# Performance work log

Hardware: AMD Instinct MI355X
Metric: run time of the kernel (lower is better)

The kernel has to match this reference:

```python
import jax, jax.numpy as jnp
import numpy as np

N_NODES = 100000
N_EDGES = 1600000
F_IN = 512
D_EMB = 128
D_HID = 64
N_CLS = 32
EPS = 1e-5


def setup_inputs() -> dict:
    key = jax.random.key(0)
    ks = jax.random.split(key, 16)
    def w(k, shape):
        fan_in = shape[0]
        return jax.random.normal(k, shape, dtype=jnp.float32) / jnp.sqrt(jnp.float32(fan_in))
    return {
        "x": jax.random.normal(ks[0], (N_NODES, F_IN), dtype=jnp.float32),
        "W1": w(ks[1], (F_IN, D_EMB)), "b1": jnp.zeros((D_EMB,), jnp.float32),
        "Wc1": w(ks[2], (D_EMB, D_HID)), "bc1": jnp.zeros((D_HID,), jnp.float32),
        "Wc2": w(ks[3], (D_HID, D_HID)), "bc2": jnp.zeros((D_HID,), jnp.float32),
        "Wc3": w(ks[4], (D_HID, D_HID)), "bc3": jnp.zeros((D_HID,), jnp.float32),
        "gamma": jnp.ones((D_HID,), jnp.float32), "beta": jnp.zeros((D_HID,), jnp.float32),
        "W2": w(ks[5], (D_HID, N_CLS)), "b2": jnp.zeros((N_CLS,), jnp.float32),
        "W3": w(ks[6], (N_CLS, N_CLS)), "b3": jnp.zeros((N_CLS,), jnp.float32),
        "edge_index": jax.random.randint(ks[7], (2, N_EDGES), 0, N_NODES, dtype=jnp.int32),
    }


def _agg_mean(h, src, dst, n):
    # gather source-node features along edges, sum into destination nodes, divide by degree
    s = jax.ops.segment_sum(h[src], dst, num_segments=n)          # [N, d]
    deg = jax.ops.segment_sum(jnp.ones((src.shape[0], 1), h.dtype), dst, num_segments=n)
    return s / jnp.maximum(deg, 1.0)


def _conv1p(h, src, dst, W, b):
    # ConvolutionalLayer_1P: neighborhood gather/aggregate -> linear -> relu
    return jax.nn.relu(_agg_mean(h, src, dst, h.shape[0]) @ W + b)


def reference(x, W1, b1, Wc1, bc1, Wc2, bc2, Wc3, bc3, gamma, beta, W2, b2, W3, b3, edge_index):
    src, dst = edge_index[0], edge_index[1]
    # linmaps1 on 0th-order ptensors == identity copy
    h = jax.nn.relu(x @ W1 + b1)                 # lin1 + relu (dropout = identity in eval)
    h = _conv1p(h, src, dst, Wc1, bc1)           # conv1
    h = _conv1p(h, src, dst, Wc2, bc2)           # conv2
    h = _conv1p(h, src, dst, Wc3, bc3)           # conv3
    mean = jnp.mean(h, axis=0)
    var = jnp.var(h, axis=0)
    h = (h - mean) * jax.lax.rsqrt(var + EPS) * gamma + beta  # batchnorm (batch stats)
    h = jax.nn.relu(h @ W2 + b2)                 # lin2 + relu (dropout = identity)
    out = h @ W3 + b3                            # lin3; linmaps0 == identity
    return out
```

## Files before the change

kernel.cpp:

```cpp
#include <hip/hip_runtime.h>
#include <cstdint>
#include <cstddef>

constexpr int F_IN  = 512;
constexpr int D_EMB = 128;
constexpr int D_HID = 64;
constexpr int N_CLS = 32;

typedef __attribute__((ext_vector_type(8))) short short8;
typedef __attribute__((ext_vector_type(4))) float floatx4;

__device__ inline unsigned short f2bf(float f) {
  union { float f; uint32_t u; } v; v.f = f;
  uint32_t r = v.u + 0x7FFF + ((v.u >> 16) & 1);
  return (unsigned short)(r >> 16);
}

__global__ __launch_bounds__(256) void wt_kernel(
    const float* __restrict__ W1, short8* __restrict__ Wt2)
{
  int idx = blockIdx.x * 256 + threadIdx.x;
  int kc8 = idx >> 10, lin = idx & 1023;
  int ct = lin >> 7, rem = lin & 127, ks = rem >> 6, ln = rem & 63;
  int col = ct * 16 + (ln & 15);
  int k0 = kc8 * 64 + ks * 32 + (ln >> 4) * 8;
  short8 s;
#pragma unroll
  for (int j = 0; j < 8; ++j)
    s[j] = (short)f2bf(W1[(size_t)(k0 + j) * D_EMB + col]);
  Wt2[idx] = s;
}

__global__ __launch_bounds__(256) void l1c1_kernel(
    const float* __restrict__ X, const short8* __restrict__ Wt2,
    const float* __restrict__ b1, const float* __restrict__ Wc1,
    float* __restrict__ P, int n)
{
  __shared__ __align__(16) char smem[50176];
  short8* Xs = (short8*)smem;
  short8* Ws = (short8*)(smem + 8192);
  float (*Hs)[132] = (float(*)[132])smem;
  float (*Wc)[64]  = (float(*)[64])(smem + 33792);

  const int t = threadIdx.x;
  const int wave = t >> 6, lane = t & 63;
  const int quad = lane >> 4, mrow = lane & 15;
  const int node0 = blockIdx.x * 64;
  const int cw = wave * 2;

  float4 wp[4];
#pragma unroll
  for (int i = 0; i < 4; ++i) wp[i] = ((const float4*)Wc1)[i * 256 + t];

  const float* sp[2];
  int soff[2];
#pragma unroll
  for (int i = 0; i < 2; ++i) {
    int g = t + i * 256;
    int row = g >> 3, col8 = g & 7;
    soff[i] = row * 128 + ((col8 * 16) ^ ((row & 7) << 4));
    int gr = node0 + row; if (gr >= n) gr = n - 1;
    sp[i] = &X[(size_t)gr * F_IN + col8 * 8];
  }

  floatx4 acc[4][2];
#pragma unroll
  for (int i = 0; i < 4; ++i)
#pragma unroll
    for (int j = 0; j < 2; ++j) acc[i][j] = (floatx4){0.f, 0.f, 0.f, 0.f};

  float4 xr[2][2];
  short8 wr[4];

#pragma unroll
  for (int i = 0; i < 2; ++i) {
    xr[i][0] = *(const float4*)sp[i];
    xr[i][1] = *(const float4*)(sp[i] + 4);
  }
#pragma unroll
  for (int i = 0; i < 4; ++i) wr[i] = Wt2[t + i * 256];

  for (int kc8 = 0; kc8 < 8; ++kc8) {
    short8 s8[2];
#pragma unroll
    for (int i = 0; i < 2; ++i) {
      s8[i][0] = (short)f2bf(xr[i][0].x); s8[i][1] = (short)f2bf(xr[i][0].y);
      s8[i][2] = (short)f2bf(xr[i][0].z); s8[i][3] = (short)f2bf(xr[i][0].w);
      s8[i][4] = (short)f2bf(xr[i][1].x); s8[i][5] = (short)f2bf(xr[i][1].y);
      s8[i][6] = (short)f2bf(xr[i][1].z); s8[i][7] = (short)f2bf(xr[i][1].w);
    }
    __syncthreads();
#pragma unroll
    for (int i = 0; i < 2; ++i)
      *(short8*)((char*)Xs + soff[i]) = s8[i];
#pragma unroll
    for (int i = 0; i < 4; ++i)
      Ws[t + i * 256] = wr[i];
    __syncthreads();

    if (kc8 < 7) {
#pragma unroll
      for (int i = 0; i < 2; ++i) {
        const float* p = sp[i] + (kc8 + 1) * 64;
        xr[i][0] = *(const float4*)p;
        xr[i][1] = *(const float4*)(p + 4);
      }
#pragma unroll
      for (int i = 0; i < 4; ++i)
        wr[i] = Wt2[(kc8 + 1) * 1024 + t + i * 256];
    }

#pragma unroll
    for (int ks = 0; ks < 2; ++ks) {
      short8 af[4], bf[2];
#pragma unroll
      for (int rt = 0; rt < 4; ++rt) {
        int row = rt * 16 + mrow;
        int byteoff = row * 128 + ((ks * 64 + quad * 16) ^ ((row & 7) << 4));
        af[rt] = *(const short8*)((const char*)Xs + byteoff);
      }
#pragma unroll
      for (int c = 0; c < 2; ++c)
        bf[c] = Ws[((cw + c) * 2 + ks) * 64 + lane];
#pragma unroll
      for (int rt = 0; rt < 4; ++rt)
#pragma unroll
        for (int c = 0; c < 2; ++c)
          acc[rt][c] = __builtin_amdgcn_mfma_f32_16x16x32_bf16(
              af[rt], bf[c], acc[rt][c], 0, 0, 0);
    }
  }

  __syncthreads();
#pragma unroll
  for (int ct = 0; ct < 2; ++ct) {
    int col = (cw + ct) * 16 + mrow;
    float b = b1[col];
#pragma unroll
    for (int rt = 0; rt < 4; ++rt)
#pragma unroll
      for (int r = 0; r < 4; ++r)
        Hs[rt * 16 + quad * 4 + r][col] = fmaxf(acc[rt][ct][r] + b, 0.f);
  }
#pragma unroll
  for (int i = 0; i < 4; ++i)
    ((float4*)&Wc[0][0])[i * 256 + t] = wp[i];
  __syncthreads();

#pragma unroll
  for (int i = 0; i < 4; ++i)
    wp[i] = ((const float4*)Wc1)[1024 + i * 256 + t];

  const int rg = t >> 4, cg = t & 15;
  float acc2[4][4];
#pragma unroll
  for (int i = 0; i < 4; ++i)
#pragma unroll
    for (int j = 0; j < 4; ++j) acc2[i][j] = 0.f;

#pragma unroll 8
  for (int k = 0; k < 64; ++k) {
    float a[4] = {Hs[rg*4+0][k], Hs[rg*4+1][k], Hs[rg*4+2][k], Hs[rg*4+3][k]};
    float4 b = *(const float4*)&Wc[k][cg * 4];
#pragma unroll
    for (int i = 0; i < 4; ++i) {
      acc2[i][0] += a[i]*b.x; acc2[i][1] += a[i]*b.y;
      acc2[i][2] += a[i]*b.z; acc2[i][3] += a[i]*b.w;
    }
  }
  __syncthreads();
#pragma unroll
  for (int i = 0; i < 4; ++i)
    ((float4*)&Wc[0][0])[i * 256 + t] = wp[i];
  __syncthreads();

#pragma unroll 8
  for (int k = 0; k < 64; ++k) {
    float a[4] = {Hs[rg*4+0][64+k], Hs[rg*4+1][64+k],
                  Hs[rg*4+2][64+k], Hs[rg*4+3][64+k]};
    float4 b = *(const float4*)&Wc[k][cg * 4];
#pragma unroll
    for (int i = 0; i < 4; ++i) {
      acc2[i][0] += a[i]*b.x; acc2[i][1] += a[i]*b.y;
      acc2[i][2] += a[i]*b.z; acc2[i][3] += a[i]*b.w;
    }
  }
#pragma unroll
  for (int i = 0; i < 4; ++i) {
    int gn = node0 + rg * 4 + i;
    if (gn < n) {
      float4 o = make_float4(acc2[i][0], acc2[i][1], acc2[i][2], acc2[i][3]);
      *(float4*)&P[(size_t)gn * 64 + cg * 4] = o;
    }
  }
}

__global__ __launch_bounds__(512) void gmm_kernel(
    const float* __restrict__ P, const int* __restrict__ offs,
    const int* __restrict__ adj, const int* __restrict__ deg,
    const float* __restrict__ bin, const float* __restrict__ W,
    float* __restrict__ Out, int n)
{
  __shared__ float Hs[64][68];
  __shared__ float Ws[64][64];
  const int t = threadIdx.x;
  const int wave = t >> 6, lane = t & 63;
  const int node0 = blockIdx.x * 64;

#pragma unroll
  for (int i = 0; i < 2; ++i) {
    int lin = t + i * 512;
    ((float4*)&Ws[0][0])[lin] = ((const float4*)W)[lin];
  }
  const float bb = bin[lane];

#pragma unroll 1
  for (int nd = 0; nd < 8; ++nd) {
    int ln = wave * 8 + nd;
    int node = node0 + ln;
    float v = 0.f;
    if (node < n) {
      int beg = offs[node], end = offs[node + 1];
      float a0 = 0.f, a1 = 0.f, a2 = 0.f, a3 = 0.f;
      int j = beg;
      while (j < end) {
        int m = min(end - j, 64);
        int idx = (lane < m) ? adj[j + lane] : 0;
        int q = 0;
        for (; q + 3 < m; q += 4) {
          int s0 = __shfl(idx, q, 64),     s1 = __shfl(idx, q + 1, 64);
          int s2 = __shfl(idx, q + 2, 64), s3 = __shfl(idx, q + 3, 64);
          a0 += P[(size_t)s0 * 64 + lane];
          a1 += P[(size_t)s1 * 64 + lane];
          a2 += P[(size_t)s2 * 64 + lane];
          a3 += P[(size_t)s3 * 64 + lane];
        }
        for (; q < m; ++q) {
          int s0 = __shfl(idx, q, 64);
          a0 += P[(size_t)s0 * 64 + lane];
        }
        j += m;
      }
      float rd = 1.f / fmaxf((float)deg[node], 1.f);
      v = fmaxf(((a0 + a2) + (a1 + a3)) * rd + bb, 0.f);
    }
    Hs[ln][lane] = v;
  }
  __syncthreads();

  const int rg = t >> 4, cg = t & 15;
  float acc[2][4];
#pragma unroll
  for (int i = 0; i < 2; ++i)
#pragma unroll
    for (int j = 0; j < 4; ++j) acc[i][j] = 0.f;

#pragma unroll 8
  for (int k = 0; k < 64; ++k) {
    float a[2] = {Hs[rg * 2 + 0][k], Hs[rg * 2 + 1][k]};
    float4 b = *(const float4*)&Ws[k][cg * 4];
#pragma unroll
    for (int i = 0; i < 2; ++i) {
      acc[i][0] += a[i]*b.x; acc[i][1] += a[i]*b.y;
      acc[i][2] += a[i]*b.z; acc[i][3] += a[i]*b.w;
    }
  }
#pragma unroll
  for (int i = 0; i < 2; ++i) {
    int gn = node0 + rg * 2 + i;
    if (gn < n) {
      float4 o = make_float4(acc[i][0], acc[i][1], acc[i][2], acc[i][3]);
      *(float4*)&Out[(size_t)gn * 64 + cg * 4] = o;
    }
  }
}

__global__ __launch_bounds__(512) void gp_kernel(
    const float* __restrict__ P, const int* __restrict__ offs,
    const int* __restrict__ adj, const int* __restrict__ deg,
    const float* __restrict__ bc3, float* __restrict__ H4,
    float* __restrict__ stats, int n)
{
  const int t = threadIdx.x;
  const int wave = t >> 6, lane = t & 63;
  const int node0 = blockIdx.x * 64;
  const float bb = bc3[lane];
  float s = 0.f, s2 = 0.f;

#pragma unroll 1
  for (int nd = 0; nd < 8; ++nd) {
    int node = node0 + wave * 8 + nd;
    if (node >= n) break;
    int beg = offs[node], end = offs[node + 1];
    float a0 = 0.f, a1 = 0.f, a2 = 0.f, a3 = 0.f;
    int j = beg;
    while (j < end) {
      int m = min(end - j, 64);
      int idx = (lane < m) ? adj[j + lane] : 0;
      int q = 0;
      for (; q + 3 < m; q += 4) {
        int s0 = __shfl(idx, q, 64),      s1 = __shfl(idx, q + 1, 64);
        int s2i = __shfl(idx, q + 2, 64), s3 = __shfl(idx, q + 3, 64);
        a0 += P[(size_t)s0 * 64 + lane];
        a1 += P[(size_t)s1 * 64 + lane];
        a2 += P[(size_t)s2i * 64 + lane];
        a3 += P[(size_t)s3 * 64 + lane];
      }
      for (; q < m; ++q) {
        int s0 = __shfl(idx, q, 64);
        a0 += P[(size_t)s0 * 64 + lane];
      }
      j += m;
    }
    float rd = 1.f / fmaxf((float)deg[node], 1.f);
    float v = fmaxf(((a0 + a2) + (a1 + a3)) * rd + bb, 0.f);
    H4[(size_t)node * 64 + lane] = v;
    s += v; s2 += v * v;
  }

  __shared__ float red[2][8][64];
  red[0][wave][lane] = s; red[1][wave][lane] = s2;
  __syncthreads();
  if (t < 128) {
    int which = t >> 6, ff = t & 63;
    float a = 0.f;
#pragma unroll
    for (int w = 0; w < 8; ++w) a += red[which][w][ff];
    atomicAdd(&stats[which * 64 + ff], a);
  }
}

__global__ __launch_bounds__(256) void hist_kernel(
    const int* __restrict__ dst, int* __restrict__ G,
    float* __restrict__ stats, int nE, int B, int NB)
{
  __shared__ int h[256];
  int blk = blockIdx.x, t = threadIdx.x;
  if (blk == 0 && t < 128) stats[t] = 0.f;
  h[t] = 0;
  __syncthreads();
  int base = blk * 8192;
  int lim = min(8192, nE - base);
  for (int i = t; i < lim; i += 256)
    atomicAdd(&h[dst[base + i] >> 9], 1);
  __syncthreads();
  if (t < NB) G[t * B + blk] = h[t];
}

__global__ __launch_bounds__(256) void scan1_kernel(
    const int* __restrict__ in, int* __restrict__ out,
    int* __restrict__ bsum, int n)
{
  __shared__ int sh[256];
  int t = threadIdx.x;
  int i = blockIdx.x * 256 + t;
  int c = (i < n) ? in[i] : 0;
  sh[t] = c;
  __syncthreads();
#pragma unroll
  for (int off = 1; off < 256; off <<= 1) {
    int v = 0;
    if (t >= off) v = sh[t - off];
    __syncthreads();
    if (t >= off) sh[t] += v;
    __syncthreads();
  }
  if (i < n) out[i] = sh[t] - c;
  if (t == 255) bsum[blockIdx.x] = sh[255];
}

__global__ __launch_bounds__(256) void scan2_kernel(int* __restrict__ bsum, int nb)
{
  __shared__ int sh[256];
  __shared__ int carry;
  int t = threadIdx.x;
  if (t == 0) carry = 0;
  __syncthreads();
  for (int base = 0; base < nb; base += 256) {
    int i = base + t;
    int v = (i < nb) ? bsum[i] : 0;
    sh[t] = v;
    __syncthreads();
#pragma unroll
    for (int off = 1; off < 256; off <<= 1) {
      int u = 0;
      if (t >= off) u = sh[t - off];
      __syncthreads();
      if (t >= off) sh[t] += u;
      __syncthreads();
    }
    int c0 = carry;
    int incl = sh[t], total = sh[255];
    if (i < nb) bsum[i] = c0 + incl - v;
    __syncthreads();
    if (t == 0) carry = c0 + total;
    __syncthreads();
  }
  if (t == 0) bsum[nb] = carry;
}

__global__ __launch_bounds__(256) void scatter2_kernel(
    const int* __restrict__ src, const int* __restrict__ dst,
    const int* __restrict__ W, const int* __restrict__ bsum,
    int2* __restrict__ EP, int nE, int B, int NB)
{
  __shared__ int cur[256];
  int blk = blockIdx.x, t = threadIdx.x;
  if (t < NB) {
    int gi = t * B + blk;
    cur[t] = W[gi] + bsum[gi >> 8];
  }
  __syncthreads();
  int base = blk * 8192;
  int lim = min(8192, nE - base);
  for (int i = t; i < lim; i += 256) {
    int s = src[base + i], d = dst[base + i];
    int slot = atomicAdd(&cur[d >> 9], 1);
    EP[slot] = make_int2(s, d);
  }
}

__global__ __launch_bounds__(256) void fillc_kernel(
    const int2* __restrict__ EP, const int* __restrict__ W,
    const int* __restrict__ bsum,
    int* __restrict__ cnt, int* __restrict__ offs, int* __restrict__ adj,
    int n, int nE, int B, int NB)
{
  __shared__ int h[512];
  int b = blockIdx.x, t = threadIdx.x;
  int g0i = b * B;
  int segStart = W[g0i] + bsum[g0i >> 8];
  int segEnd = (b == NB - 1) ? nE : (W[g0i + B] + bsum[(g0i + B) >> 8]);
  int nodeBase = b << 9;

  h[t] = 0; h[t + 256] = 0;
  __syncthreads();
  for (int i = segStart + t; i < segEnd; i += 256)
    atomicAdd(&h[EP[i].y - nodeBase], 1);
  __syncthreads();
  int c0 = h[t], c1 = h[t + 256];
#pragma unroll
  for (int off = 1; off < 512; off <<= 1) {
    int a = (t >= off) ? h[t - off] : 0;
    int bb = (t + 256 >= off) ? h[t + 256 - off] : 0;
    __syncthreads();
    h[t] += a; h[t + 256] += bb;
    __syncthreads();
  }
  int e0 = h[t] - c0, e1 = h[t + 256] - c1;
  int g0 = nodeBase + t, g1 = nodeBase + t + 256;
  if (g0 < n) { cnt[g0] = c0; offs[g0] = segStart + e0; }
  if (g1 < n) { cnt[g1] = c1; offs[g1] = segStart + e1; }
  if (b == 0 && t == 0) offs[n] = nE;
  __syncthreads();
  h[t] = e0; h[t + 256] = e1;
  __syncthreads();
  for (int i = segStart + t; i < segEnd; i += 256) {
    int2 p = EP[i];
    int slot = atomicAdd(&h[p.y - nodeBase], 1);
    adj[segStart + slot] = p.x;
  }
}

__global__ __launch_bounds__(256) void fold_kernel(
    const float* __restrict__ stats, const float* __restrict__ gamma,
    const float* __restrict__ beta, const float* __restrict__ W2,
    const float* __restrict__ b2, float* __restrict__ W2f,
    float* __restrict__ b2f, int n)
{
  __shared__ float rsg[64], corr[64];
  int t = threadIdx.x;
  if (t < 64) {
    float m = stats[t] / (float)n;
    float var = stats[64 + t] / (float)n - m * m;
    float rs = rsqrtf(var + 1e-5f);
    float g = gamma[t] * rs;
    rsg[t] = g;
    corr[t] = beta[t] - m * g;
  }
  __syncthreads();
#pragma unroll
  for (int i = 0; i < 8; ++i) {
    int lin = t + i * 256;
    int k = lin >> 5;
    W2f[lin] = rsg[k] * W2[lin];
  }
  if (t < 32) {
    float a = b2[t];
    for (int k = 0; k < 64; ++k) a += corr[k] * W2[k * 32 + t];
    b2f[t] = a;
  }
}

__global__ __launch_bounds__(256) void final_kernel(
    const float* __restrict__ H4, const float* __restrict__ W2f,
    const float* __restrict__ b2f, const float* __restrict__ W3,
    const float* __restrict__ b3, float* __restrict__ Out, int n)
{
  __shared__ float Hs[64][68];
  __shared__ float W2s[64][32];
  __shared__ float W3s[32][32];
  __shared__ float Us[64][36];
  __shared__ float b2s[32], b3s[32];
  const int t = threadIdx.x;
  const int node0 = blockIdx.x * 64;

#pragma unroll
  for (int i = 0; i < 4; ++i) {
    int lin = t + i * 256;
    int node = lin >> 4, kq = lin & 15;
    float4 v = make_float4(0.f, 0.f, 0.f, 0.f);
    if (node0 + node < n)
      v = *(const float4*)&H4[(size_t)(node0 + node) * 64 + kq * 4];
    *(float4*)&Hs[node][kq * 4] = v;
  }
#pragma unroll
  for (int i = 0; i < 2; ++i) {
    int lin = t + i * 256;
    ((float4*)&W2s[0][0])[lin] = ((const float4*)W2f)[lin];
  }
  ((float4*)&W3s[0][0])[t & 255] = ((const float4*)W3)[t & 255];
  if (t < 32) { b2s[t] = b2f[t]; b3s[t] = b3[t]; }
  __syncthreads();

  const int rg = t >> 4, cg = t & 15;
  float acc[4][2] = {{0.f,0.f},{0.f,0.f},{0.f,0.f},{0.f,0.f}};
#pragma unroll 8
  for (int k = 0; k < 64; ++k) {
    float a[4] = {Hs[rg*4+0][k], Hs[rg*4+1][k], Hs[rg*4+2][k], Hs[rg*4+3][k]};
    float w0 = W2s[k][cg*2], w1 = W2s[k][cg*2+1];
#pragma unroll
    for (int i = 0; i < 4; ++i) { acc[i][0] += a[i]*w0; acc[i][1] += a[i]*w1; }
  }
#pragma unroll
  for (int i = 0; i < 4; ++i) {
    Us[rg*4+i][cg*2+0] = fmaxf(acc[i][0] + b2s[cg*2+0], 0.f);
    Us[rg*4+i][cg*2+1] = fmaxf(acc[i][1] + b2s[cg*2+1], 0.f);
  }
  __syncthreads();

  float acc2[4][2] = {{0.f,0.f},{0.f,0.f},{0.f,0.f},{0.f,0.f}};
#pragma unroll
  for (int k = 0; k < 32; ++k) {
    float a[4] = {Us[rg*4+0][k], Us[rg*4+1][k], Us[rg*4+2][k], Us[rg*4+3][k]};
    float w0 = W3s[k][cg*2], w1 = W3s[k][cg*2+1];
#pragma unroll
    for (int i = 0; i < 4; ++i) { acc2[i][0] += a[i]*w0; acc2[i][1] += a[i]*w1; }
  }
  float (*Os)[36] = (float(*)[36])Hs;
#pragma unroll
  for (int i = 0; i < 4; ++i) {
    Os[rg*4+i][cg*2+0] = acc2[i][0] + b3s[cg*2+0];
    Os[rg*4+i][cg*2+1] = acc2[i][1] + b3s[cg*2+1];
  }
  __syncthreads();
#pragma unroll
  for (int i = 0; i < 2; ++i) {
    int lin = t + i * 256;
    int node = lin >> 3, c4 = lin & 7;
    if (node0 + node < n)
      *(float4*)&Out[(size_t)(node0 + node) * 32 + c4 * 4] =
          *(float4*)&Os[node][c4 * 4];
  }
}

extern "C" void kernel_launch(void* const* d_in, const int* in_sizes, int n_in,
                              void* d_out, int out_size, void* d_ws, size_t ws_size,
                              hipStream_t stream)
{
  const float* X     = (const float*)d_in[0];
  const float* W1    = (const float*)d_in[1];
  const float* b1    = (const float*)d_in[2];
  const float* Wc1   = (const float*)d_in[3];
  const float* bc1   = (const float*)d_in[4];
  const float* Wc2   = (const float*)d_in[5];
  const float* bc2   = (const float*)d_in[6];
  const float* Wc3   = (const float*)d_in[7];
  const float* bc3   = (const float*)d_in[8];
  const float* gamma = (const float*)d_in[9];
  const float* beta  = (const float*)d_in[10];
  const float* W2    = (const float*)d_in[11];
  const float* b2    = (const float*)d_in[12];
  const float* W3    = (const float*)d_in[13];
  const float* b3    = (const float*)d_in[14];
  const int*   ei    = (const int*)d_in[15];

  const int n  = in_sizes[0] / F_IN;
  const int nE = in_sizes[15] / 2;
  const int* src  = ei;
  const int* dstv = ei + nE;

  const int NB = (n + 511) >> 9;
  const int B  = (nE + 8191) >> 13;
  const int NG = NB * B;
  const int nbG = (NG + 255) / 256;

  float* ws    = (float*)d_ws;
  float* Pa    = ws;
  float* Pb    = Pa + (size_t)n * D_HID;
  float* stats = Pb + (size_t)n * D_HID;
  float* W2f   = stats + 128;
  float* b2f   = W2f + 2048;
  int*   cnt   = (int*)(b2f + 32);
  int*   offs  = cnt + n;
  int*   G     = offs + n + 1;
  int*   W     = G + NG;
  int*   bsum  = W + NG + 1;
  int*   adj   = bsum + nbG + 1;
  uintptr_t epAddr = ((uintptr_t)(adj + nE) + 7) & ~(uintptr_t)7;
  int2*  EP    = (int2*)epAddr;
  short8* Wt2  = (short8*)(EP + nE);
  float* H4    = Pb;

  const int nb  = (n + 63) / 64;

  wt_kernel<<<32, 256, 0, stream>>>(W1, Wt2);
  l1c1_kernel<<<nb, 256, 0, stream>>>(X, Wt2, b1, Wc1, Pa, n);

  hist_kernel<<<B, 256, 0, stream>>>(dstv, G, stats, nE, B, NB);
  scan1_kernel<<<nbG, 256, 0, stream>>>(G, W, bsum, NG);
  scan2_kernel<<<1, 256, 0, stream>>>(bsum, nbG);
  scatter2_kernel<<<B, 256, 0, stream>>>(src, dstv, W, bsum, EP, nE, B, NB);
  fillc_kernel<<<NB, 256, 0, stream>>>(EP, W, bsum, cnt, offs, adj, n, nE, B, NB);

  gmm_kernel<<<nb, 512, 0, stream>>>(Pa, offs, adj, cnt, bc1, Wc2, Pb, n);

  gmm_kernel<<<nb, 512, 0, stream>>>(Pb, offs, adj, cnt, bc2, Wc3, Pa, n);

  gp_kernel<<<nb, 512, 0, stream>>>(Pa, offs, adj, cnt, bc3, H4, stats, n);

  fold_kernel<<<1, 256, 0, stream>>>(stats, gamma, beta, W2, b2, W2f, b2f, n);
  final_kernel<<<nb, 256, 0, stream>>>(H4, W2f, b2f, W3, b3, (float*)d_out, n);
}
```

Baseline: 657.8 us.

## Double-buffer lin1 GEMM prefetch and unroll neighbor gather with scalar index loads

The lin1 bf16 MFMA GEMM now keeps two register prefetch buffers, so global loads for K-chunk k+2 are issued while chunk k is computed, which hides more load latency at the cost of extra registers. The neighbor-aggregation loops in gmm_kernel and gp_kernel are replaced by a shared gather_row helper. It reads edge indices as wave-uniform values through readfirstlane on the offsets, and keeps eight independent loads in flight with a masked tail instead of using shuffles. This removes shuffle overhead and raises memory-level parallelism in the gathers, but the tail block can issue up to seven redundant loads.

```diff
diff --git a/kernel.cpp b/kernel.cpp
--- a/kernel.cpp
+++ b/kernel.cpp
@@ -69,18 +69,23 @@
 #pragma unroll
     for (int j = 0; j < 2; ++j) acc[i][j] = (floatx4){0.f, 0.f, 0.f, 0.f};
 
-  float4 xr[2][2];
-  short8 wr[4];
+  float4 xrA[2][2], xrB[2][2];
+  short8 wrA[4], wrB[4];
 
 #pragma unroll
   for (int i = 0; i < 2; ++i) {
-    xr[i][0] = *(const float4*)sp[i];
-    xr[i][1] = *(const float4*)(sp[i] + 4);
-  }
-#pragma unroll
-  for (int i = 0; i < 4; ++i) wr[i] = Wt2[t + i * 256];
-
-  for (int kc8 = 0; kc8 < 8; ++kc8) {
+    xrA[i][0] = *(const float4*)sp[i];
+    xrA[i][1] = *(const float4*)(sp[i] + 4);
+    xrB[i][0] = *(const float4*)(sp[i] + 64);
+    xrB[i][1] = *(const float4*)(sp[i] + 68);
+  }
+#pragma unroll
+  for (int i = 0; i < 4; ++i) {
+    wrA[i] = Wt2[t + i * 256];
+    wrB[i] = Wt2[1024 + t + i * 256];
+  }
+
+  auto substep = [&](float4 (&xr)[2][2], short8 (&wr)[4], int knext) {
     short8 s8[2];
 #pragma unroll
     for (int i = 0; i < 2; ++i) {
@@ -98,16 +103,16 @@
       Ws[t + i * 256] = wr[i];
     __syncthreads();
 
-    if (kc8 < 7) {
+    if (knext < 8) {
 #pragma unroll
       for (int i = 0; i < 2; ++i) {
-        const float* p = sp[i] + (kc8 + 1) * 64;
+        const float* p = sp[i] + knext * 64;
         xr[i][0] = *(const float4*)p;
         xr[i][1] = *(const float4*)(p + 4);
       }
 #pragma unroll
       for (int i = 0; i < 4; ++i)
-        wr[i] = Wt2[(kc8 + 1) * 1024 + t + i * 256];
+        wr[i] = Wt2[knext * 1024 + t + i * 256];
     }
 
 #pragma unroll
@@ -129,6 +134,12 @@
           acc[rt][c] = __builtin_amdgcn_mfma_f32_16x16x32_bf16(
               af[rt], bf[c], acc[rt][c], 0, 0, 0);
     }
+  };
+
+#pragma unroll 1
+  for (int kc8 = 0; kc8 < 8; kc8 += 2) {
+    substep(xrA, wrA, kc8 + 2);
+    substep(xrB, wrB, kc8 + 3);
   }
 
   __syncthreads();
@@ -193,6 +204,47 @@
       *(float4*)&P[(size_t)gn * 64 + cg * 4] = o;
     }
   }
+}
+
+__device__ inline float gather_row(
+    const float* __restrict__ P, const int* __restrict__ adj,
+    int beg, int end, int lane)
+{
+  float a0=0.f,a1=0.f,a2=0.f,a3=0.f,a4=0.f,a5=0.f,a6=0.f,a7=0.f;
+  int j = beg;
+  for (; j + 8 <= end; j += 8) {
+    int s0=adj[j+0], s1=adj[j+1], s2=adj[j+2], s3=adj[j+3];
+    int s4=adj[j+4], s5=adj[j+5], s6=adj[j+6], s7=adj[j+7];
+    a0 += P[(size_t)s0 * 64 + lane];
+    a1 += P[(size_t)s1 * 64 + lane];
+    a2 += P[(size_t)s2 * 64 + lane];
+    a3 += P[(size_t)s3 * 64 + lane];
+    a4 += P[(size_t)s4 * 64 + lane];
+    a5 += P[(size_t)s5 * 64 + lane];
+    a6 += P[(size_t)s6 * 64 + lane];
+    a7 += P[(size_t)s7 * 64 + lane];
+  }
+  if (j < end) {
+    int e1 = end - 1;
+    int s0 = adj[j];
+    int s1 = adj[min(j+1,e1)], s2 = adj[min(j+2,e1)], s3 = adj[min(j+3,e1)];
+    int s4 = adj[min(j+4,e1)], s5 = adj[min(j+5,e1)], s6 = adj[min(j+6,e1)];
+    float v0 = P[(size_t)s0 * 64 + lane];
+    float v1 = P[(size_t)s1 * 64 + lane];
+    float v2 = P[(size_t)s2 * 64 + lane];
+    float v3 = P[(size_t)s3 * 64 + lane];
+    float v4 = P[(size_t)s4 * 64 + lane];
+    float v5 = P[(size_t)s5 * 64 + lane];
+    float v6 = P[(size_t)s6 * 64 + lane];
+    a0 += v0;
+    a1 += (j+1 < end) ? v1 : 0.f;
+    a2 += (j+2 < end) ? v2 : 0.f;
+    a3 += (j+3 < end) ? v3 : 0.f;
+    a4 += (j+4 < end) ? v4 : 0.f;
+    a5 += (j+5 < end) ? v5 : 0.f;
+    a6 += (j+6 < end) ? v6 : 0.f;
+  }
+  return ((a0+a1)+(a2+a3))+((a4+a5)+(a6+a7));
 }
 
 __global__ __launch_bounds__(512) void gmm_kernel(
@@ -220,29 +272,11 @@
     int node = node0 + ln;
     float v = 0.f;
     if (node < n) {
-      int beg = offs[node], end = offs[node + 1];
-      float a0 = 0.f, a1 = 0.f, a2 = 0.f, a3 = 0.f;
-      int j = beg;
-      while (j < end) {
-        int m = min(end - j, 64);
-        int idx = (lane < m) ? adj[j + lane] : 0;
-        int q = 0;
-        for (; q + 3 < m; q += 4) {
-          int s0 = __shfl(idx, q, 64),     s1 = __shfl(idx, q + 1, 64);
-          int s2 = __shfl(idx, q + 2, 64), s3 = __shfl(idx, q + 3, 64);
-          a0 += P[(size_t)s0 * 64 + lane];
-          a1 += P[(size_t)s1 * 64 + lane];
-          a2 += P[(size_t)s2 * 64 + lane];
-          a3 += P[(size_t)s3 * 64 + lane];
-        }
-        for (; q < m; ++q) {
-          int s0 = __shfl(idx, q, 64);
-          a0 += P[(size_t)s0 * 64 + lane];
-        }
-        j += m;
-      }
+      int beg = __builtin_amdgcn_readfirstlane(offs[node]);
+      int end = __builtin_amdgcn_readfirstlane(offs[node + 1]);
+      float s = gather_row(P, adj, beg, end, lane);
       float rd = 1.f / fmaxf((float)deg[node], 1.f);
-      v = fmaxf(((a0 + a2) + (a1 + a3)) * rd + bb, 0.f);
+      v = fmaxf(s * rd + bb, 0.f);
     }
     Hs[ln][lane] = v;
   }
@@ -291,29 +325,11 @@
   for (int nd = 0; nd < 8; ++nd) {
     int node = node0 + wave * 8 + nd;
     if (node >= n) break;
-    int beg = offs[node], end = offs[node + 1];
-    float a0 = 0.f, a1 = 0.f, a2 = 0.f, a3 = 0.f;
-    int j = beg;
-    while (j < end) {
-      int m = min(end - j, 64);
-      int idx = (lane < m) ? adj[j + lane] : 0;
-      int q = 0;
-      for (; q + 3 < m; q += 4) {
-        int s0 = __shfl(idx, q, 64),      s1 = __shfl(idx, q + 1, 64);
-        int s2i = __shfl(idx, q + 2, 64), s3 = __shfl(idx, q + 3, 64);
-        a0 += P[(size_t)s0 * 64 + lane];
-        a1 += P[(size_t)s1 * 64 + lane];
-        a2 += P[(size_t)s2i * 64 + lane];
-        a3 += P[(size_t)s3 * 64 + lane];
-      }
-      for (; q < m; ++q) {
-        int s0 = __shfl(idx, q, 64);
-        a0 += P[(size_t)s0 * 64 + lane];
-      }
-      j += m;
-    }
+    int beg = __builtin_amdgcn_readfirstlane(offs[node]);
+    int end = __builtin_amdgcn_readfirstlane(offs[node + 1]);
+    float a = gather_row(P, adj, beg, end, lane);
     float rd = 1.f / fmaxf((float)deg[node], 1.f);
-    float v = fmaxf(((a0 + a2) + (a1 + a3)) * rd + bb, 0.f);
+    float v = fmaxf(a * rd + bb, 0.f);
     H4[(size_t)node * 64 + lane] = v;
     s += v; s2 += v * v;
   }
```

Result: faster. 632.0 us (-3.9%).
